# Optimization experiments

Hardware: AMD Instinct MI355X
Metric: run time of the kernel (lower is better)

Reference implementation:

```python
import jax, jax.numpy as jnp
import numpy as np

LRELU_ALPHA = 0.2       # LeakyReLU slope (alpha arg of GraphAttentionLayer)
NEG_INF = -9e15         # zero_vec value from the torch code
N1, N2, N3 = 3000, 2500, 2500
IN_F, OUT_F, HEADS = 128, 64, 2


def setup_inputs() -> dict:
    key = jax.random.key(0)
    ks = jax.random.split(key, 13)
    N = N1 + N2 + N3
    h = jax.random.normal(ks[0], (N, IN_F), jnp.float32)
    A1  = jax.random.randint(ks[1],  (N1, N1), 0, 2, jnp.int32)
    A2  = jax.random.randint(ks[2],  (N2, N2), 0, 2, jnp.int32)
    A3  = jax.random.randint(ks[3],  (N3, N3), 0, 2, jnp.int32)
    A12 = jax.random.randint(ks[4],  (N1, N2), 0, 2, jnp.int32)
    A13 = jax.random.randint(ks[5],  (N1, N3), 0, 2, jnp.int32)
    A23 = jax.random.randint(ks[6],  (N2, N3), 0, 2, jnp.int32)
    A21 = jax.random.randint(ks[7],  (N2, N1), 0, 2, jnp.int32)
    A31 = jax.random.randint(ks[8],  (N3, N1), 0, 2, jnp.int32)
    A32 = jax.random.randint(ks[9],  (N3, N2), 0, 2, jnp.int32)
    # per-head GAT parameters (xavier-ish scale)
    Ws = jax.random.normal(ks[10], (HEADS, IN_F, OUT_F), jnp.float32) * 0.12
    a_param = jax.random.normal(ks[11], (HEADS, 2 * OUT_F, 1), jnp.float32) * 0.12
    return dict(h=h, A1=A1, A2=A2, A3=A3, A12=A12, A13=A13, A23=A23,
                A21=A21, A31=A31, A32=A32, Ws=Ws, a_param=a_param)


def reference(h, A1, A2, A3, A12, A13, A23, A21, A31, A32, Ws, a_param):
    n1, n2, n3 = A1.shape[0], A2.shape[0], A3.shape[0]
    # The 9 block assignments in the torch forward tile the full NxN matrix,
    # so they are equivalent to one block-structured mask.
    mask = jnp.block([[A1,  A12, A13],
                      [A21, A2,  A23],
                      [A31, A32, A3]]) > 0          # [N, N] bool

    Wh = jnp.einsum('nf,hfo->hno', h, Ws)           # [H, N, O]
    a1 = a_param[:, :OUT_F, 0]                      # [H, O]
    a2 = a_param[:, OUT_F:, 0]                      # [H, O]
    Wh1 = jnp.einsum('hno,ho->hn', Wh, a1)          # [H, N]
    Wh2 = jnp.einsum('hno,ho->hn', Wh, a2)          # [H, N]
    e = jax.nn.leaky_relu(Wh1[:, :, None] + Wh2[:, None, :], LRELU_ALPHA)  # [H,N,N]
    att = jax.nn.softmax(jnp.where(mask[None], e, NEG_INF), axis=-1)
    # dropout is identity in eval mode
    mid = jnp.einsum('hij,hjo->hio', att, Wh)       # [H, N, O]
    out = jax.nn.elu(mid)                           # concat=True -> elu
    x2 = out.transpose(1, 0, 2).reshape(h.shape[0], -1)  # [N, H*O] head concat

    x3 = jax.nn.log_softmax(x2[n1 + n2:], axis=1)   # group-3 nodes
    x4 = jax.nn.log_softmax(x2[:n1], axis=1)        # group-1 nodes
    x5 = jax.nn.log_softmax(x2[n1:n1 + n2], axis=1) # group-2 nodes
    return (x3, x4, x5)
```

## Files before the change

### kernel.cpp

```cpp
#include <hip/hip_runtime.h>
#include <hip/hip_bf16.h>


#define CN1 3000
#define CN2 2500
#define CN3 2500
#define NTOT 8000
#define INF_ 128
#define OUTF 64
#define LOG2E 1.44269504088896340736f
#define ALPHA 0.2f

typedef __attribute__((ext_vector_type(4))) float f32x4;
typedef __attribute__((ext_vector_type(8))) short short8;
union B16x8 { int4 i4; short8 s8; unsigned int u[4]; };

#if defined(__has_builtin)
#if __has_builtin(__builtin_amdgcn_exp2f)
#define EXP2F(x) __builtin_amdgcn_exp2f(x)
#endif
#endif
#ifndef EXP2F
#define EXP2F(x) exp2f(x)
#endif

__device__ inline float wave_sum(float v) {
  for (int d = 32; d; d >>= 1) v += __shfl_xor(v, d, 64);
  return v;
}

__device__ inline unsigned int pack2_bf16(float a, float b) {
  unsigned ua = __float_as_uint(a);
  ua = (ua + 0x7FFFu + ((ua >> 16) & 1u)) >> 16;
  unsigned ub = __float_as_uint(b);
  ub = (ub + 0x7FFFu + ((ub >> 16) & 1u)) & 0xFFFF0000u;
  return ub | ua;
}

__global__ __launch_bounds__(256)
void k_pack(const int* __restrict__ A1,  const int* __restrict__ A12, const int* __restrict__ A13,
            const int* __restrict__ A21, const int* __restrict__ A2,  const int* __restrict__ A23,
            const int* __restrict__ A31, const int* __restrict__ A32, const int* __restrict__ A3,
            unsigned int* __restrict__ packed) {
  const int i = blockIdx.x * 4 + (threadIdx.x >> 6);
  const int lane = threadIdx.x & 63;
  const int *p0, *p1, *p2;
  if (i < CN1)            { p0 = A1  + i * CN1;          p1 = A12 + i * CN2;          p2 = A13 + i * CN3; }
  else if (i < CN1 + CN2) { int r = i - CN1;       p0 = A21 + r * CN1; p1 = A2  + r * CN2; p2 = A23 + r * CN3; }
  else                    { int r = i - CN1 - CN2; p0 = A31 + r * CN1; p1 = A32 + r * CN2; p2 = A3  + r * CN3; }
  unsigned int* pkrow = packed + (i >> 4) * 4000 + (i & 15);
  for (int cb = 0; cb < 5; ++cb) {
    int v[25];
#pragma unroll
    for (int u = 0; u < 25; ++u) {
      const int j = (cb * 25 + u) * 64 + lane;
      v[u] = (j < CN1) ? p0[j]
           : (j < CN1 + CN2) ? p1[j - CN1]
                             : p2[j - CN1 - CN2];
    }
#pragma unroll
    for (int u = 0; u < 25; ++u) {
      unsigned long long bm = __ballot(v[u] > 0);
      const int c = cb * 25 + u;
      if (lane == 0) {
        pkrow[(2 * c) * 16]     = (unsigned int)(bm & 0xffffffffull);
        pkrow[(2 * c + 1) * 16] = (unsigned int)(bm >> 32);
      }
    }
  }
}

__global__ void k_wh(const float* __restrict__ hv, const float* __restrict__ Wsv,
                     const float* __restrict__ ap,
                     float* __restrict__ Whf,
                     float* __restrict__ Wh1s,
                     float* __restrict__ Wh2s) {
  const int t = threadIdx.x;
  const int o = t & 63;
  const int n = blockIdx.x * 2 + (t >> 6);
  const float* hrow = hv + n * INF_;
  const float* Ws0 = Wsv + o;
  const float* Ws1 = Wsv + INF_ * OUTF + o;
  float a0a = 0.f, a0b = 0.f, a1a = 0.f, a1b = 0.f;
#pragma unroll 8
  for (int f = 0; f < INF_; f += 2) {
    float h0 = hrow[f], h1 = hrow[f + 1];
    a0a += h0 * Ws0[f * OUTF];
    a0b += h1 * Ws0[(f + 1) * OUTF];
    a1a += h0 * Ws1[f * OUTF];
    a1b += h1 * Ws1[(f + 1) * OUTF];
  }
  float acc0 = a0a + a0b, acc1 = a1a + a1b;
  Whf[(0 * NTOT + n) * OUTF + o] = acc0;
  Whf[(1 * NTOT + n) * OUTF + o] = acc1;
  float s10 = wave_sum(acc0 * ap[o]);
  float s20 = wave_sum(acc0 * ap[OUTF + o]);
  float s11 = wave_sum(acc1 * ap[2 * OUTF + o]);
  float s21 = wave_sum(acc1 * ap[3 * OUTF + o]);
  if (o == 0) {
    Wh1s[n] = s10 * LOG2E;        Wh2s[n] = s20 * LOG2E;
    Wh1s[NTOT + n] = s11 * LOG2E; Wh2s[NTOT + n] = s21 * LOG2E;
  }
}

__global__ void k_m2(const float* __restrict__ Wh2s, float* __restrict__ M2s) {
  const int hd = blockIdx.x;
  float mx = -1e30f;
  for (int i = threadIdx.x; i < NTOT; i += 256)
    mx = fmaxf(mx, Wh2s[hd * NTOT + i]);
  for (int d = 32; d; d >>= 1) mx = fmaxf(mx, __shfl_xor(mx, d, 64));
  __shared__ float red[4];
  if ((threadIdx.x & 63) == 0) red[threadIdx.x >> 6] = mx;
  __syncthreads();
  if (threadIdx.x == 0)
    M2s[hd] = fmaxf(fmaxf(red[0], red[1]), fmaxf(red[2], red[3]));
}

__global__ void k_bpack(const float* __restrict__ Whf, int4* __restrict__ WhB) {
  const int gid = blockIdx.x * 256 + threadIdx.x;
  const int lane = gid & 63;
  const int c = (gid >> 6) & 3;
  const int t = (gid >> 8) % 250;
  const int hd = gid / 64000;
  const int jb = t * 32 + (lane >> 4) * 8;
  const int col = c * 16 + (lane & 15);
  const float* src = Whf + (hd * NTOT + jb) * OUTF + col;
  B16x8 out;
#pragma unroll
  for (int e2 = 0; e2 < 4; ++e2)
    out.u[e2] = pack2_bf16(src[(2 * e2) * OUTF], src[(2 * e2 + 1) * OUTF]);
  WhB[gid] = out.i4;
}

__global__ __launch_bounds__(128, 2)
void k_attn_mfma(const unsigned int* __restrict__ packed,
                 const float* __restrict__ Wh1s, const float* __restrict__ Wh2s,
                 const float* __restrict__ M2s, const int4* __restrict__ WhB,
                 float* __restrict__ partAcc,
                 float* __restrict__ partS)
{
  const int widx = threadIdx.x >> 6;
  const int lane = threadIdx.x & 63;
  const int m = lane & 15;
  const int g = lane >> 4;
  const int kb = g * 8;
  const int rowblk = blockIdx.x * 2 + widx;
  const int i = rowblk * 16 + m;
  const int jy = blockIdx.y, njy = gridDim.y;
  const int t0 = (250 * jy) / njy, t1 = (250 * (jy + 1)) / njy;

  const unsigned int* pkb = packed + rowblk * 4000 + m;

  const float w1s0 = Wh1s[i],        w1s1 = Wh1s[NTOT + i];
  const float y0 = w1s0 + M2s[0],    y1 = w1s1 + M2s[1];
  const float ci0 = fmaxf(y0, ALPHA * y0), ci1 = fmaxf(y1, ALPHA * y1);
  const float a1c0 = w1s0 - ci0, b1c0 = ALPHA * w1s0 - ci0;
  const float a1c1 = w1s1 - ci1, b1c1 = ALPHA * w1s1 - ci1;
  const float* wh2_0 = Wh2s;
  const float* wh2_1 = Wh2s + NTOT;

  f32x4 a0_0 = {0.f,0.f,0.f,0.f}, a0_1 = a0_0, a0_2 = a0_0, a0_3 = a0_0;
  f32x4 a1_0 = a0_0, a1_1 = a0_0, a1_2 = a0_0, a1_3 = a0_0;
  float sp0 = 0.f, sp1 = 0.f;

  struct Frags { int4 f0[4], f1[4]; float4 w0a, w0b, w1a, w1b; };
  auto load_frags = [&](int t, Frags& F) {
    const int4* bp0 = WhB + t * 256 + lane;
    const int4* bp1 = WhB + (250 + t) * 256 + lane;
#pragma unroll
    for (int c = 0; c < 4; ++c) { F.f0[c] = bp0[c * 64]; F.f1[c] = bp1[c * 64]; }
    const float* w0 = wh2_0 + t * 32 + kb;
    const float* w1 = wh2_1 + t * 32 + kb;
    F.w0a = *(const float4*)w0; F.w0b = *(const float4*)(w0 + 4);
    F.w1a = *(const float4*)w1; F.w1b = *(const float4*)(w1 + 4);
  };

  auto compute = [&](unsigned int mw, const Frags& F) {
    const unsigned bits = (mw >> kb) & 0xffu;
    const float w0v[8] = {F.w0a.x, F.w0a.y, F.w0a.z, F.w0a.w, F.w0b.x, F.w0b.y, F.w0b.z, F.w0b.w};
    const float w1v[8] = {F.w1a.x, F.w1a.y, F.w1a.z, F.w1a.w, F.w1b.x, F.w1b.y, F.w1b.z, F.w1b.w};
    float q0[8], q1[8];
#pragma unroll
    for (int e = 0; e < 8; ++e) {
      bool on = ((bits >> e) & 1u) != 0u;
      float xa0 = a1c0 + w0v[e];
      float xb0 = fmaf(ALPHA, w0v[e], b1c0);
      float p0e = EXP2F(fmaxf(xa0, xb0));
      q0[e] = on ? p0e : 0.f;
      float xa1 = a1c1 + w1v[e];
      float xb1 = fmaf(ALPHA, w1v[e], b1c1);
      float p1e = EXP2F(fmaxf(xa1, xb1));
      q1[e] = on ? p1e : 0.f;
    }
    sp0 += ((q0[0] + q0[1]) + (q0[2] + q0[3])) + ((q0[4] + q0[5]) + (q0[6] + q0[7]));
    sp1 += ((q1[0] + q1[1]) + (q1[2] + q1[3])) + ((q1[4] + q1[5]) + (q1[6] + q1[7]));
    B16x8 af0, af1;
#pragma unroll
    for (int e2 = 0; e2 < 4; ++e2) {
      af0.u[e2] = pack2_bf16(q0[2 * e2], q0[2 * e2 + 1]);
      af1.u[e2] = pack2_bf16(q1[2 * e2], q1[2 * e2 + 1]);
    }
    B16x8 b;
    b.i4 = F.f0[0]; a0_0 = __builtin_amdgcn_mfma_f32_16x16x32_bf16(af0.s8, b.s8, a0_0, 0, 0, 0);
    b.i4 = F.f0[1]; a0_1 = __builtin_amdgcn_mfma_f32_16x16x32_bf16(af0.s8, b.s8, a0_1, 0, 0, 0);
    b.i4 = F.f0[2]; a0_2 = __builtin_amdgcn_mfma_f32_16x16x32_bf16(af0.s8, b.s8, a0_2, 0, 0, 0);
    b.i4 = F.f0[3]; a0_3 = __builtin_amdgcn_mfma_f32_16x16x32_bf16(af0.s8, b.s8, a0_3, 0, 0, 0);
    b.i4 = F.f1[0]; a1_0 = __builtin_amdgcn_mfma_f32_16x16x32_bf16(af1.s8, b.s8, a1_0, 0, 0, 0);
    b.i4 = F.f1[1]; a1_1 = __builtin_amdgcn_mfma_f32_16x16x32_bf16(af1.s8, b.s8, a1_1, 0, 0, 0);
    b.i4 = F.f1[2]; a1_2 = __builtin_amdgcn_mfma_f32_16x16x32_bf16(af1.s8, b.s8, a1_2, 0, 0, 0);
    b.i4 = F.f1[3]; a1_3 = __builtin_amdgcn_mfma_f32_16x16x32_bf16(af1.s8, b.s8, a1_3, 0, 0, 0);
  };

  unsigned int mw0 = pkb[t0 * 16];
  unsigned int mw1 = pkb[min(t0 + 1, t1 - 1) * 16];
  Frags Fc, Fn;
  load_frags(t0, Fc);
  for (int t = t0; t < t1; ++t) {
    load_frags(min(t + 1, t1 - 1), Fn);
    unsigned int mw2 = pkb[min(t + 2, t1 - 1) * 16];
    compute(mw0, Fc);
    mw0 = mw1; mw1 = mw2;
    Fc = Fn;
  }

  sp0 += __shfl_xor(sp0, 16, 64); sp0 += __shfl_xor(sp0, 32, 64);
  sp1 += __shfl_xor(sp1, 16, 64); sp1 += __shfl_xor(sp1, 32, 64);
  const int base0 = (jy * 2 + 0) * NTOT + rowblk * 16;
  const int base1 = (jy * 2 + 1) * NTOT + rowblk * 16;
  if (lane < 16) {
    partS[base0 + lane] = sp0;
    partS[base1 + lane] = sp1;
  }

  float* o0 = partAcc + base0 * OUTF;
  float* o1 = partAcc + base1 * OUTF;
#pragma unroll
  for (int q = 0; q < 4; ++q) {
    const int row = g * 4 + q;
    o0[row * OUTF +      m] = a0_0[q];
    o0[row * OUTF + 16 + m] = a0_1[q];
    o0[row * OUTF + 32 + m] = a0_2[q];
    o0[row * OUTF + 48 + m] = a0_3[q];
    o1[row * OUTF +      m] = a1_0[q];
    o1[row * OUTF + 16 + m] = a1_1[q];
    o1[row * OUTF + 32 + m] = a1_2[q];
    o1[row * OUTF + 48 + m] = a1_3[q];
  }
}

__global__ void k_final(const float* __restrict__ partAcc, const float* __restrict__ partS,
                        int njy, float* __restrict__ out) {
  const int wave = threadIdx.x >> 6, lane = threadIdx.x & 63;
  const int n = blockIdx.x * 4 + wave;
  float x[2];
#pragma unroll
  for (int hd = 0; hd < 2; ++hd) {
    float a = 0.f, s = 0.f;
    for (int jy = 0; jy < njy; ++jy) {
      a += partAcc[((jy * 2 + hd) * NTOT + n) * OUTF + lane];
      s += partS[(jy * 2 + hd) * NTOT + n];
    }
    float mid = a / s;
    x[hd] = mid > 0.f ? mid : (__expf(mid) - 1.f);
  }
  float mx = fmaxf(x[0], x[1]);
  for (int d = 32; d; d >>= 1) mx = fmaxf(mx, __shfl_xor(mx, d, 64));
  float se = __expf(x[0] - mx) + __expf(x[1] - mx);
  for (int d = 32; d; d >>= 1) se += __shfl_xor(se, d, 64);
  const float lse = mx + __logf(se);
  const int orow = (n >= CN1 + CN2) ? (n - CN1 - CN2) : (n + CN3);
  out[orow * 128 + lane]      = x[0] - lse;
  out[orow * 128 + 64 + lane] = x[1] - lse;
}

__global__ void k_sentinel(float* __restrict__ out, float v) {
  out[blockIdx.x * 256 + threadIdx.x] = v;
}

extern "C" void kernel_launch(void* const* d_in, const int* in_sizes, int n_in,
                              void* d_out, int out_size, void* d_ws, size_t ws_size,
                              hipStream_t stream) {
  float* outf = (float*)d_out;

  static const int EXP[12] = {1024000, 9000000, 6250000, 6250000, 7500000, 7500000,
                              6250000, 7500000, 7500000, 6250000, 16384, 256};
  bool exact = (n_in == 12);
  if (exact) for (int i = 0; i < 12; ++i) if (in_sizes[i] != EXP[i]) { exact = false; break; }

  const size_t FIXED = 64000 + 64000 + 256 + 2048000 + 8000000;
  int njy = 0;
  for (int cand = 4; cand >= 1; cand >>= 1) {
    size_t need = FIXED + (size_t)cand * 64000 + (size_t)cand * 4096000;
    if (ws_size >= need) { njy = cand; break; }
  }
  if (!exact || njy == 0) {
    k_sentinel<<<dim3(4000), dim3(256), 0, stream>>>(outf, -148.0f);
    return;
  }

  const float* h  = (const float*)d_in[0];
  const int* A1  = (const int*)d_in[1];
  const int* A2  = (const int*)d_in[2];
  const int* A3  = (const int*)d_in[3];
  const int* A12 = (const int*)d_in[4];
  const int* A13 = (const int*)d_in[5];
  const int* A23 = (const int*)d_in[6];
  const int* A21 = (const int*)d_in[7];
  const int* A31 = (const int*)d_in[8];
  const int* A32 = (const int*)d_in[9];
  const float* Ws = (const float*)d_in[10];
  const float* ap = (const float*)d_in[11];

  char* w = (char*)d_ws;
  float*        Wh1s    = (float*)(w);
  float*        Wh2s    = (float*)(w + 64000);
  float*        M2s     = (float*)(w + 128000);
  int4*         WhB     = (int4*) (w + 128256);
  unsigned int* packed  = (unsigned int*)(w + 2176256);
  float*        partS   = (float*)(w + 10176256);
  float*        Whf     = (float*)(w + 10176256 + (size_t)njy * 64000);
  float*        partAcc = Whf;

  k_pack     <<<dim3(2000),     dim3(256), 0, stream>>>(A1, A12, A13, A21, A2, A23, A31, A32, A3,
                                                        packed);
  k_wh       <<<dim3(4000),     dim3(128), 0, stream>>>(h, Ws, ap, Whf, Wh1s, Wh2s);
  k_m2       <<<dim3(2),        dim3(256), 0, stream>>>(Wh2s, M2s);
  k_bpack    <<<dim3(500),      dim3(256), 0, stream>>>(Whf, WhB);
  k_attn_mfma<<<dim3(250, njy), dim3(128), 0, stream>>>(packed, Wh1s, Wh2s, M2s, WhB,
                                                        partAcc, partS);
  k_final    <<<dim3(2000),     dim3(256), 0, stream>>>(partAcc, partS, njy, outf);
}
```

Measured before the change: 397.2 us.

## Split K across two waves per block, row sums via MFMA, LDS reduction

```diff
diff --git a/kernel.cpp b/kernel.cpp
--- a/kernel.cpp
+++ b/kernel.cpp
@@ -27,6 +27,12 @@
 __device__ inline float wave_sum(float v) {
   for (int d = 32; d; d >>= 1) v += __shfl_xor(v, d, 64);
   return v;
+}
+
+__device__ inline unsigned int pk2(float a, float b) {
+  union { __hip_bfloat162 h; unsigned int u; } cv;
+  cv.h = __float22bfloat162_rn(make_float2(a, b));
+  return cv.u;
 }
 
 __device__ inline unsigned int pack2_bf16(float a, float b) {
@@ -132,7 +138,7 @@
   WhB[gid] = out.i4;
 }
 
-__global__ __launch_bounds__(128, 2)
+__global__ __launch_bounds__(128)
 void k_attn_mfma(const unsigned int* __restrict__ packed,
                  const float* __restrict__ Wh1s, const float* __restrict__ Wh2s,
                  const float* __restrict__ M2s, const int4* __restrict__ WhB,
@@ -144,10 +150,11 @@
   const int m = lane & 15;
   const int g = lane >> 4;
   const int kb = g * 8;
-  const int rowblk = blockIdx.x * 2 + widx;
+  const int rowblk = blockIdx.x;
   const int i = rowblk * 16 + m;
   const int jy = blockIdx.y, njy = gridDim.y;
-  const int t0 = (250 * jy) / njy, t1 = (250 * (jy + 1)) / njy;
+  const int s = jy * 2 + widx, ns = njy * 2;
+  const int t0 = (250 * s) / ns, t1 = (250 * (s + 1)) / ns;
 
   const unsigned int* pkb = packed + rowblk * 4000 + m;
 
@@ -161,7 +168,11 @@
 
   f32x4 a0_0 = {0.f,0.f,0.f,0.f}, a0_1 = a0_0, a0_2 = a0_0, a0_3 = a0_0;
   f32x4 a1_0 = a0_0, a1_1 = a0_0, a1_2 = a0_0, a1_3 = a0_0;
-  float sp0 = 0.f, sp1 = 0.f;
+  f32x4 s0v = a0_0, s1v = a0_0;
+
+  B16x8 ones;
+#pragma unroll
+  for (int e2 = 0; e2 < 4; ++e2) ones.u[e2] = 0x3F803F80u;
 
   struct Frags { int4 f0[4], f1[4]; float4 w0a, w0b, w1a, w1b; };
   auto load_frags = [&](int t, Frags& F) {
@@ -192,23 +203,23 @@
       float p1e = EXP2F(fmaxf(xa1, xb1));
       q1[e] = on ? p1e : 0.f;
     }
-    sp0 += ((q0[0] + q0[1]) + (q0[2] + q0[3])) + ((q0[4] + q0[5]) + (q0[6] + q0[7]));
-    sp1 += ((q1[0] + q1[1]) + (q1[2] + q1[3])) + ((q1[4] + q1[5]) + (q1[6] + q1[7]));
     B16x8 af0, af1;
 #pragma unroll
     for (int e2 = 0; e2 < 4; ++e2) {
-      af0.u[e2] = pack2_bf16(q0[2 * e2], q0[2 * e2 + 1]);
-      af1.u[e2] = pack2_bf16(q1[2 * e2], q1[2 * e2 + 1]);
+      af0.u[e2] = pk2(q0[2 * e2], q0[2 * e2 + 1]);
+      af1.u[e2] = pk2(q1[2 * e2], q1[2 * e2 + 1]);
     }
     B16x8 b;
     b.i4 = F.f0[0]; a0_0 = __builtin_amdgcn_mfma_f32_16x16x32_bf16(af0.s8, b.s8, a0_0, 0, 0, 0);
     b.i4 = F.f0[1]; a0_1 = __builtin_amdgcn_mfma_f32_16x16x32_bf16(af0.s8, b.s8, a0_1, 0, 0, 0);
     b.i4 = F.f0[2]; a0_2 = __builtin_amdgcn_mfma_f32_16x16x32_bf16(af0.s8, b.s8, a0_2, 0, 0, 0);
     b.i4 = F.f0[3]; a0_3 = __builtin_amdgcn_mfma_f32_16x16x32_bf16(af0.s8, b.s8, a0_3, 0, 0, 0);
+    s0v = __builtin_amdgcn_mfma_f32_16x16x32_bf16(af0.s8, ones.s8, s0v, 0, 0, 0);
     b.i4 = F.f1[0]; a1_0 = __builtin_amdgcn_mfma_f32_16x16x32_bf16(af1.s8, b.s8, a1_0, 0, 0, 0);
     b.i4 = F.f1[1]; a1_1 = __builtin_amdgcn_mfma_f32_16x16x32_bf16(af1.s8, b.s8, a1_1, 0, 0, 0);
     b.i4 = F.f1[2]; a1_2 = __builtin_amdgcn_mfma_f32_16x16x32_bf16(af1.s8, b.s8, a1_2, 0, 0, 0);
     b.i4 = F.f1[3]; a1_3 = __builtin_amdgcn_mfma_f32_16x16x32_bf16(af1.s8, b.s8, a1_3, 0, 0, 0);
+    s1v = __builtin_amdgcn_mfma_f32_16x16x32_bf16(af1.s8, ones.s8, s1v, 0, 0, 0);
   };
 
   unsigned int mw0 = pkb[t0 * 16];
@@ -223,28 +234,41 @@
     Fc = Fn;
   }
 
-  sp0 += __shfl_xor(sp0, 16, 64); sp0 += __shfl_xor(sp0, 32, 64);
-  sp1 += __shfl_xor(sp1, 16, 64); sp1 += __shfl_xor(sp1, 32, 64);
-  const int base0 = (jy * 2 + 0) * NTOT + rowblk * 16;
-  const int base1 = (jy * 2 + 1) * NTOT + rowblk * 16;
-  if (lane < 16) {
-    partS[base0 + lane] = sp0;
-    partS[base1 + lane] = sp1;
-  }
-
-  float* o0 = partAcc + base0 * OUTF;
-  float* o1 = partAcc + base1 * OUTF;
-#pragma unroll
-  for (int q = 0; q < 4; ++q) {
-    const int row = g * 4 + q;
-    o0[row * OUTF +      m] = a0_0[q];
-    o0[row * OUTF + 16 + m] = a0_1[q];
-    o0[row * OUTF + 32 + m] = a0_2[q];
-    o0[row * OUTF + 48 + m] = a0_3[q];
-    o1[row * OUTF +      m] = a1_0[q];
-    o1[row * OUTF + 16 + m] = a1_1[q];
-    o1[row * OUTF + 32 + m] = a1_2[q];
-    o1[row * OUTF + 48 + m] = a1_3[q];
+  __shared__ f32x4 lds[10][64];
+  if (widx == 1) {
+    lds[0][lane] = a0_0; lds[1][lane] = a0_1; lds[2][lane] = a0_2; lds[3][lane] = a0_3;
+    lds[4][lane] = a1_0; lds[5][lane] = a1_1; lds[6][lane] = a1_2; lds[7][lane] = a1_3;
+    lds[8][lane] = s0v;  lds[9][lane] = s1v;
+  }
+  __syncthreads();
+  if (widx == 0) {
+    a0_0 += lds[0][lane]; a0_1 += lds[1][lane]; a0_2 += lds[2][lane]; a0_3 += lds[3][lane];
+    a1_0 += lds[4][lane]; a1_1 += lds[5][lane]; a1_2 += lds[6][lane]; a1_3 += lds[7][lane];
+    s0v  += lds[8][lane]; s1v  += lds[9][lane];
+
+    const int base0 = (jy * 2 + 0) * NTOT + rowblk * 16;
+    const int base1 = (jy * 2 + 1) * NTOT + rowblk * 16;
+    if (m == 0) {
+#pragma unroll
+      for (int q = 0; q < 4; ++q) {
+        partS[base0 + g * 4 + q] = s0v[q];
+        partS[base1 + g * 4 + q] = s1v[q];
+      }
+    }
+    float* o0 = partAcc + base0 * OUTF;
+    float* o1 = partAcc + base1 * OUTF;
+#pragma unroll
+    for (int q = 0; q < 4; ++q) {
+      const int row = g * 4 + q;
+      o0[row * OUTF +      m] = a0_0[q];
+      o0[row * OUTF + 16 + m] = a0_1[q];
+      o0[row * OUTF + 32 + m] = a0_2[q];
+      o0[row * OUTF + 48 + m] = a0_3[q];
+      o1[row * OUTF +      m] = a1_0[q];
+      o1[row * OUTF + 16 + m] = a1_1[q];
+      o1[row * OUTF + 32 + m] = a1_2[q];
+      o1[row * OUTF + 48 + m] = a1_3[q];
+    }
   }
 }
 
@@ -289,7 +313,7 @@
 
   const size_t FIXED = 64000 + 64000 + 256 + 2048000 + 8000000;
   int njy = 0;
-  for (int cand = 4; cand >= 1; cand >>= 1) {
+  for (int cand = 8; cand >= 1; cand >>= 1) {
     size_t need = FIXED + (size_t)cand * 64000 + (size_t)cand * 4096000;
     if (ws_size >= need) { njy = cand; break; }
   }
@@ -326,7 +350,7 @@
   k_wh       <<<dim3(4000),     dim3(128), 0, stream>>>(h, Ws, ap, Whf, Wh1s, Wh2s);
   k_m2       <<<dim3(2),        dim3(256), 0, stream>>>(Wh2s, M2s);
   k_bpack    <<<dim3(500),      dim3(256), 0, stream>>>(Whf, WhB);
-  k_attn_mfma<<<dim3(250, njy), dim3(128), 0, stream>>>(packed, Wh1s, Wh2s, M2s, WhB,
+  k_attn_mfma<<<dim3(500, njy), dim3(128), 0, stream>>>(packed, Wh1s, Wh2s, M2s, WhB,
                                                         partAcc, partS);
   k_final    <<<dim3(2000),     dim3(256), 0, stream>>>(partAcc, partS, njy, outf);
 }
```

After: 363.4 us. 8.5% less time.
